# Optimization experiments

Measured on AMD Instinct MI355X. Metric: run time of the kernel, lower is better.

The kernel has to match this reference:

```python
import jax, jax.numpy as jnp
import numpy as np
from jax import lax

B, N, C = 8, 2000, 81
MAX_INST = 100
MIN_CONF = 0.7
NMS_THR = 0.3
WINDOW = jnp.array([0.0, 0.0, 1.0, 1.0], jnp.float32)  # y1, x1, y2, x2
BBOX_STD = jnp.array([0.1, 0.1, 0.2, 0.2], jnp.float32)


def setup_inputs() -> dict:
    key = jax.random.key(0)
    k1, k2, k3 = jax.random.split(key, 3)
    # build valid boxes: sample coordinate pairs and sort so y1<=y2, x1<=x2
    yx = jax.random.uniform(k1, (B, N, 2, 2), dtype=jnp.float32)
    mins, maxs = yx.min(axis=2), yx.max(axis=2)
    rois = jnp.stack([mins[..., 0], mins[..., 1], maxs[..., 0], maxs[..., 1]], axis=-1)
    probs = jax.random.uniform(k2, (B, N, C), dtype=jnp.float32)
    deltas = jax.random.normal(k3, (B, N, C, 4), dtype=jnp.float32) * 0.5
    return {"rois": rois, "probs": probs, "deltas": deltas}


def _apply_box_deltas(boxes, deltas):
    # boxes: [N,4] (y1,x1,y2,x2); deltas: [N,4] (dy,dx,log_dh,log_dw)
    h = boxes[:, 2] - boxes[:, 0]
    w = boxes[:, 3] - boxes[:, 1]
    cy = boxes[:, 0] + 0.5 * h + deltas[:, 0] * h
    cx = boxes[:, 1] + 0.5 * w + deltas[:, 1] * w
    h = h * jnp.exp(deltas[:, 2])
    w = w * jnp.exp(deltas[:, 3])
    return jnp.stack([cy - 0.5 * h, cx - 0.5 * w, cy + 0.5 * h, cx + 0.5 * w], axis=1)


def _clip_boxes(boxes, window):
    wy1, wx1, wy2, wx2 = window
    y1 = jnp.clip(boxes[:, 0], wy1, wy2)
    x1 = jnp.clip(boxes[:, 1], wx1, wx2)
    y2 = jnp.clip(boxes[:, 2], wy1, wy2)
    x2 = jnp.clip(boxes[:, 3], wx1, wx2)
    return jnp.stack([y1, x1, y2, x2], axis=1)


def _pairwise_iou(boxes):
    # boxes: [N,4] -> [N,N]
    y1, x1, y2, x2 = boxes[:, 0], boxes[:, 1], boxes[:, 2], boxes[:, 3]
    area = (y2 - y1) * (x2 - x1)
    iy1 = jnp.maximum(y1[:, None], y1[None, :])
    ix1 = jnp.maximum(x1[:, None], x1[None, :])
    iy2 = jnp.minimum(y2[:, None], y2[None, :])
    ix2 = jnp.minimum(x2[:, None], x2[None, :])
    inter = jnp.maximum(iy2 - iy1, 0.0) * jnp.maximum(ix2 - ix1, 0.0)
    union = area[:, None] + area[None, :] - inter
    return inter / jnp.maximum(union, 1e-12)


def _refine_one(rois, probs, deltas):
    # rois [N,4], probs [N,C], deltas [N,C,4]
    class_ids = jnp.argmax(probs, axis=1)                      # [N]
    rng = jnp.arange(N)
    class_scores = probs[rng, class_ids]                       # [N]
    deltas_specific = deltas[rng, class_ids]                   # [N,4]
    refined = _apply_box_deltas(rois, deltas_specific * BBOX_STD)
    refined = _clip_boxes(refined, WINDOW)

    valid = (class_ids > 0) & (class_scores >= MIN_CONF)

    # sort by score descending (invalid entries pushed to the end)
    order = jnp.argsort(-jnp.where(valid, class_scores, -jnp.inf))
    boxes_s = refined[order]
    scores_s = class_scores[order]
    cls_s = class_ids[order]
    valid_s = valid[order]

    # per-class greedy NMS: suppress only within the same class
    iou = _pairwise_iou(boxes_s)                               # [N,N]
    suppress_mat = (iou > NMS_THR) & (cls_s[:, None] == cls_s[None, :])
    lower = jnp.arange(N)

    def body(i, keep):
        sup = suppress_mat[i] & keep[i] & (lower > i)
        return keep & ~sup

    keep = lax.fori_loop(0, N, body, valid_s)

    # per-class cap at MAX_INST (mirrors max_output_size in tf NMS)
    onehot = jax.nn.one_hot(cls_s, C, dtype=jnp.int32) * keep.astype(jnp.int32)[:, None]
    rank = jnp.cumsum(onehot, axis=0)[lower, cls_s]            # inclusive per-class rank
    keep = keep & (rank <= MAX_INST)

    # global top-k by score among kept, zero-padded
    final_scores = jnp.where(keep, scores_s, -jnp.inf)
    _, top_idx = lax.top_k(final_scores, MAX_INST)
    valid_top = keep[top_idx]
    box_out = jnp.where(valid_top[:, None], boxes_s[top_idx], 0.0)
    cls_out = jnp.where(valid_top, cls_s[top_idx].astype(jnp.float32), 0.0)
    sc_out = jnp.where(valid_top, scores_s[top_idx], 0.0)
    return jnp.concatenate([box_out, cls_out[:, None], sc_out[:, None]], axis=1)  # [MAX_INST,6]


def reference(rois, probs, deltas):
    return jax.vmap(_refine_one)(rois, probs, deltas)  # [B, MAX_INST, 6]
```

## Files before the change

kernel.cpp:

```cpp
#include <hip/hip_runtime.h>
#include <math.h>

#define BB 8
#define NN 2000
#define CC 81
#define NCLS 80
#define MAXI 100
#define MCLS 128
#define WCAP 128

static constexpr float kMinConf = 0.7f;
static constexpr float kNmsThr  = 0.3f;


__device__ __forceinline__ unsigned long long mkey(float s, int i) {
    return ((unsigned long long)__float_as_uint(s) << 32) | (unsigned int)(~(unsigned int)i);
}

__device__ __forceinline__ bool iou_gt_thr(float4 a, float aarea, float4 t) {
    float iy1 = fmaxf(a.x, t.x), ix1 = fmaxf(a.y, t.y);
    float iy2 = fminf(a.z, t.z), ix2 = fminf(a.w, t.w);
    float inter = fmaxf(iy2 - iy1, 0.f) * fmaxf(ix2 - ix1, 0.f);
    float tarea = (t.z - t.x) * (t.w - t.y);
    float uni = fmaxf(aarea + tarea - inter, 1e-12f);
    return inter > kNmsThr * uni;
}

__global__ void kA_refine(const float* __restrict__ rois,
                          const float* __restrict__ probs,
                          const float* __restrict__ deltas,
                          float* __restrict__ boxes,
                          float* __restrict__ sc,
                          int* __restrict__ cls,
                          int* __restrict__ kflag,
                          float* __restrict__ outz) {
    int gtid = blockIdx.x * blockDim.x + threadIdx.x;
    if (gtid < BB * MAXI * 6) outz[gtid] = 0.f;
    if (gtid < BB * NN) kflag[gtid] = 0;

    int wid = gtid >> 6;
    int l = gtid & 63;

    const float* p = probs + (size_t)wid * CC;
    float v1 = p[l];
    int   i1 = l;
    int   c2 = l + 64;
    float v2 = (c2 < CC) ? p[c2] : -1.0f;
    float bv; int bi;
    if (v2 > v1) { bv = v2; bi = c2; } else { bv = v1; bi = i1; }

    #pragma unroll
    for (int off = 32; off; off >>= 1) {
        float ov = __shfl_xor(bv, off);
        int   oi = __shfl_xor(bi, off);
        if (ov > bv || (ov == bv && oi < bi)) { bv = ov; bi = oi; }
    }

    if (l == 0) {
        const float4 dl = *(const float4*)(deltas + ((size_t)wid * CC + bi) * 4);
        float dy = dl.x * 0.1f, dx = dl.y * 0.1f, dh = dl.z * 0.2f, dw = dl.w * 0.2f;
        const float4 r = *(const float4*)(rois + (size_t)wid * 4);
        float y1 = r.x, x1 = r.y, y2 = r.z, x2 = r.w;
        float h = y2 - y1, w = x2 - x1;
        float cy = y1 + 0.5f * h + dy * h;
        float cx = x1 + 0.5f * w + dx * w;
        float h2 = h * expf(dh);
        float w2 = w * expf(dw);
        float oy1 = fminf(fmaxf(cy - 0.5f * h2, 0.f), 1.f);
        float ox1 = fminf(fmaxf(cx - 0.5f * w2, 0.f), 1.f);
        float oy2 = fminf(fmaxf(cy + 0.5f * h2, 0.f), 1.f);
        float ox2 = fminf(fmaxf(cx + 0.5f * w2, 0.f), 1.f);
        bool valid = (bi > 0) && (bv >= kMinConf);
        float4 bx; bx.x = oy1; bx.y = ox1; bx.z = oy2; bx.w = ox2;
        ((float4*)boxes)[wid] = bx;
        sc[wid] = bv;
        cls[wid] = valid ? bi : 0;
    }
}

__global__ void __launch_bounds__(256) kB_nms(
        const float* __restrict__ boxes,
        const float* __restrict__ sc,
        const int* __restrict__ cls,
        int* __restrict__ kflag) {
    const int p = blockIdx.x;
    const int b = p / NCLS;
    const int cidx = p % NCLS;
    const int c = cidx + 1;
    const int tid = threadIdx.x;
    const int wv = tid >> 6;
    const int l = tid & 63;

    __shared__ unsigned long long wlist[4][WCAP];
    __shared__ int wcnt[4];
    __shared__ unsigned long long mk[MCLS];
    __shared__ float4 mbox[MCLS];

    const int* cl = cls + (size_t)b * NN;
    const float* ssc = sc + (size_t)b * NN;
    const float4* bxs = (const float4*)boxes + (size_t)b * NN;

    {
        int cnt = 0;
        const int base_row = wv * 500;
        for (int ch = 0; ch < 8; ++ch) {
            int idx = ch * 64 + l;
            bool inq = idx < 500;
            int r = base_row + idx;
            int ci = inq ? cl[r] : 0;
            bool pred = (ci == c);
            unsigned long long mask = __ballot(pred);
            if (pred) {
                int pos = cnt + __popcll(mask & ((1ull << l) - 1ull));
                if (pos < WCAP) wlist[wv][pos] = mkey(ssc[r], r);
            }
            cnt += __popcll(mask);
        }
        if (l == 0) wcnt[wv] = (cnt > WCAP) ? WCAP : cnt;
    }
    __syncthreads();

    int b0 = wcnt[0], b1 = wcnt[1], b2 = wcnt[2], b3 = wcnt[3];
    int myofs = (wv > 0 ? b0 : 0) + (wv > 1 ? b1 : 0) + (wv > 2 ? b2 : 0);
    int myn = wcnt[wv];
    int cnt_all = b0 + b1 + b2 + b3;
    if (cnt_all > MCLS) cnt_all = MCLS;
    if (l < myn && myofs + l < MCLS) mk[myofs + l] = wlist[wv][l];
    if (64 + l < myn && myofs + 64 + l < MCLS) mk[myofs + 64 + l] = wlist[wv][64 + l];
    __syncthreads();

    if (wv != 0) return;
    if (cnt_all == 0) return;
    const int cnt = cnt_all;

    {
        unsigned long long Ka = (l < cnt) ? mk[l] : 0ull;
        unsigned long long Kb = (64 + l < cnt) ? mk[64 + l] : 0ull;
        int ra = 0, rb = 0;
        for (int t = 0; t < cnt; ++t) {
            unsigned long long kt = mk[t];
            ra += (kt > Ka);
            rb += (kt > Kb);
        }
        if (l < cnt) mk[ra] = Ka;
        if (64 + l < cnt) mk[rb] = Kb;
    }

    for (int t = l; t < cnt; t += 64) {
        int i = (int)(~(unsigned int)mk[t]);
        mbox[t] = bxs[i];
    }

    unsigned long long kept0 = 0ull;
    {
        bool act = (l < cnt);
        float4 a = mbox[act ? l : 0];
        float aarea = (a.z - a.x) * (a.w - a.y);
        unsigned long long colmask = 0ull;
        int tend = min(64, cnt);
        for (int t = 0; t < tend; ++t) {
            float4 tb = mbox[t];
            if (t < l && act && iou_gt_thr(a, aarea, tb)) colmask |= (1ull << t);
        }
        unsigned long long kept = __ballot(act);
        while (true) {
            bool alive = act && ((colmask & kept) == 0ull);
            unsigned long long k2m = __ballot(alive);
            if (k2m == kept) break;
            kept = k2m;
        }
        kept0 = kept;
        bool alive = act && ((colmask & kept0) == 0ull);
        if (alive) kflag[(size_t)b * NN + (int)(~(unsigned int)mk[l])] = 1;
    }
    if (cnt > 64) {
        int m = 64 + l;
        bool act = (m < cnt);
        float4 a = mbox[act ? m : 0];
        float aarea = (a.z - a.x) * (a.w - a.y);
        bool presup = false;
        for (int t = 0; t < 64; ++t) {
            if ((kept0 >> t) & 1ull) {
                if (act && iou_gt_thr(a, aarea, mbox[t])) presup = true;
            }
        }
        unsigned long long colmask = 0ull;
        for (int t = 64; t < cnt; ++t) {
            float4 tb = mbox[t];
            if ((t - 64) < l && act && iou_gt_thr(a, aarea, tb)) colmask |= (1ull << (t - 64));
        }
        bool pre = act && !presup;
        unsigned long long kept = __ballot(pre);
        while (true) {
            bool alive = pre && ((colmask & kept) == 0ull);
            unsigned long long k2m = __ballot(alive);
            if (k2m == kept) break;
            kept = k2m;
        }
        bool alive = pre && ((colmask & kept) == 0ull);
        if (alive) kflag[(size_t)b * NN + (int)(~(unsigned int)mk[64 + l])] = 1;
    }
}

__global__ void __launch_bounds__(1024) kC_emit(
        const int* __restrict__ kflag,
        const float* __restrict__ sc,
        const float* __restrict__ boxes,
        const int* __restrict__ cls,
        float* __restrict__ out) {
    const int b = blockIdx.x;
    const int tid = threadIdx.x;
    const int wv = tid >> 6;
    const int l = tid & 63;

    __shared__ unsigned long long keys[2048];
    __shared__ ulonglong2 cand2[256];
    __shared__ int hist[256];
    __shared__ int Tcnt, tbsh, candn;
    unsigned long long* cand = (unsigned long long*)cand2;

    if (tid < 256) hist[tid] = 0;
    if (tid < 48) keys[2000 + tid] = 0ull;
    if (tid == 0) { Tcnt = 0; candn = 0; }
    __syncthreads();

    for (int i = tid; i < NN; i += 1024) {
        int f = kflag[(size_t)b * NN + i];
        unsigned long long k = f ? mkey(sc[(size_t)b * NN + i], i) : 0ull;
        keys[i] = k;
        if (f) atomicAdd(&hist[(int)((k >> 47) & 0xFF)], 1);
        unsigned long long m = __ballot(f != 0);
        if (l == 0 && m) atomicAdd(&Tcnt, __popcll(m));
    }
    __syncthreads();
    const int T = Tcnt;
    if (T == 0) return;

    if (wv == 0) {
        int cum = 0, tb = 0, done = 0;
        for (int chunk = 3; chunk >= 0 && !done; --chunk) {
            int bkt = chunk * 64 + (63 - l);
            int s = hist[bkt];
            #pragma unroll
            for (int off = 1; off < 64; off <<= 1) {
                int o = __shfl_up(s, off);
                if (l >= off) s += o;
            }
            int chunktot = __shfl(s, 63);
            if (cum + chunktot >= MAXI) {
                unsigned long long m = __ballot(cum + s >= MAXI);
                int lane = __ffsll((long long)m) - 1;
                tb = chunk * 64 + (63 - lane);
                done = 1;
            } else {
                cum += chunktot;
            }
        }
        if (l == 0) tbsh = done ? tb : 0;
    }
    __syncthreads();
    const int tb = tbsh;

    for (int i = tid; i < NN; i += 1024) {
        unsigned long long k = keys[i];
        bool pr = (k != 0ull) && ((int)((k >> 47) & 0xFF) >= tb);
        unsigned long long m = __ballot(pr);
        int basew = 0;
        if (l == 0 && m) basew = atomicAdd(&candn, __popcll(m));
        basew = __shfl(basew, 0);
        if (pr) {
            int pos = basew + __popcll(m & ((1ull << l) - 1ull));
            if (pos < 512) cand[pos] = k;
        }
    }
    __syncthreads();
    const int nc = candn;
    if (tid == 0 && nc < 512) cand[nc] = 0ull;
    __syncthreads();

    if (nc <= 512) {
        const int np = (nc + 1) >> 1;
        for (int s = tid; s < nc; s += 1024) {
            unsigned long long myk = cand[s];
            int r = 0;
            for (int t = 0; t < np; ++t) {
                ulonglong2 kv = cand2[t];
                r += (int)(kv.x > myk);
                r += (int)(kv.y > myk);
            }
            if (r < MAXI) {
                int i = (int)(~(unsigned int)myk);
                float4 bx = ((const float4*)boxes)[(size_t)b * NN + i];
                float* o = out + ((size_t)b * MAXI + r) * 6;
                o[0] = bx.x; o[1] = bx.y; o[2] = bx.z; o[3] = bx.w;
                o[4] = (float)cls[(size_t)b * NN + i];
                o[5] = __uint_as_float((unsigned int)(myk >> 32));
            }
        }
    } else {
        for (int s = tid; s < NN; s += 1024) {
            unsigned long long myk = keys[s];
            if (myk == 0ull) continue;
            int r = 0;
            for (int t = 0; t < 1024; ++t) {
                ulonglong2 kv = ((ulonglong2*)keys)[t];
                r += (int)(kv.x > myk);
                r += (int)(kv.y > myk);
            }
            if (r < MAXI) {
                int i = (int)(~(unsigned int)myk);
                float4 bx = ((const float4*)boxes)[(size_t)b * NN + i];
                float* o = out + ((size_t)b * MAXI + r) * 6;
                o[0] = bx.x; o[1] = bx.y; o[2] = bx.z; o[3] = bx.w;
                o[4] = (float)cls[(size_t)b * NN + i];
                o[5] = __uint_as_float((unsigned int)(myk >> 32));
            }
        }
    }
}

extern "C" void kernel_launch(void* const* d_in, const int* in_sizes, int n_in,
                              void* d_out, int out_size, void* d_ws, size_t ws_size,
                              hipStream_t stream) {
    const float* rois   = (const float*)d_in[0];
    const float* probs  = (const float*)d_in[1];
    const float* deltas = (const float*)d_in[2];
    float* outp = (float*)d_out;

    char* ws = (char*)d_ws;
    float* boxes = (float*)(ws + 0);
    float* sc    = (float*)(ws + 256000);
    int*   cls   = (int*)  (ws + 320000);
    int*   kflag = (int*)  (ws + 384000);

    {
        int blocks = (BB * NN * 64) / 256;
        kA_refine<<<blocks, 256, 0, stream>>>(rois, probs, deltas, boxes, sc, cls, kflag, outp);
    }
    {
        kB_nms<<<BB * NCLS, 256, 0, stream>>>(boxes, sc, cls, kflag);
    }
    {
        kC_emit<<<BB, 1024, 0, stream>>>(kflag, sc, boxes, cls, outp);
    }
}
```

Measured before the change: 29.09 us.

## Bucket detections per class via atomics and fuse NMS with emit kernel

The refine kernel now appends each valid detection's score/index key into per-class slot lists using atomic counters. This replaces the NMS kernel's full scan of class ids. NMS and top-k emission are fused into one 1024-thread block per batch, with 16 wavefronts each handling 5 classes and writing kept keys straight into shared memory instead of a global flag array. This removes a kernel launch and global round-trips, but adds a memset, atomic contention, and far fewer blocks (8 instead of 640) for the NMS work.

```diff
diff --git a/kernel.cpp b/kernel.cpp
--- a/kernel.cpp
+++ b/kernel.cpp
@@ -7,7 +7,6 @@
 #define NCLS 80
 #define MAXI 100
 #define MCLS 128
-#define WCAP 128
 
 static constexpr float kMinConf = 0.7f;
 static constexpr float kNmsThr  = 0.3f;
@@ -30,13 +29,12 @@
                           const float* __restrict__ probs,
                           const float* __restrict__ deltas,
                           float* __restrict__ boxes,
-                          float* __restrict__ sc,
                           int* __restrict__ cls,
-                          int* __restrict__ kflag,
+                          int* __restrict__ ccnt,
+                          unsigned long long* __restrict__ cslot,
                           float* __restrict__ outz) {
     int gtid = blockIdx.x * blockDim.x + threadIdx.x;
     if (gtid < BB * MAXI * 6) outz[gtid] = 0.f;
-    if (gtid < BB * NN) kflag[gtid] = 0;
 
     int wid = gtid >> 6;
     int l = gtid & 63;
@@ -73,170 +71,136 @@
         bool valid = (bi > 0) && (bv >= kMinConf);
         float4 bx; bx.x = oy1; bx.y = ox1; bx.z = oy2; bx.w = ox2;
         ((float4*)boxes)[wid] = bx;
-        sc[wid] = bv;
         cls[wid] = valid ? bi : 0;
-    }
-}
-
-__global__ void __launch_bounds__(256) kB_nms(
+        if (valid) {
+            int b = wid / NN, i = wid - b * NN;
+            int cidx = bi - 1;
+            int pos = atomicAdd(&ccnt[b * NCLS + cidx], 1);
+            if (pos < MCLS)
+                cslot[(size_t)(b * NCLS + cidx) * MCLS + pos] = mkey(bv, i);
+        }
+    }
+}
+
+__global__ void __launch_bounds__(1024) k2_nms_emit(
         const float* __restrict__ boxes,
-        const float* __restrict__ sc,
         const int* __restrict__ cls,
-        int* __restrict__ kflag) {
-    const int p = blockIdx.x;
-    const int b = p / NCLS;
-    const int cidx = p % NCLS;
-    const int c = cidx + 1;
+        const int* __restrict__ ccnt,
+        const unsigned long long* __restrict__ cslot,
+        float* __restrict__ out) {
+    const int b = blockIdx.x;
     const int tid = threadIdx.x;
-    const int wv = tid >> 6;
+    const int w = tid >> 6;
     const int l = tid & 63;
 
-    __shared__ unsigned long long wlist[4][WCAP];
-    __shared__ int wcnt[4];
-    __shared__ unsigned long long mk[MCLS];
-    __shared__ float4 mbox[MCLS];
-
-    const int* cl = cls + (size_t)b * NN;
-    const float* ssc = sc + (size_t)b * NN;
+    __shared__ unsigned long long mk16[16][MCLS];
+    __shared__ float4 mbox16[16][64];
+    __shared__ ulonglong2 keys2[1024];
+    __shared__ ulonglong2 cand2[256];
+    __shared__ int hist[256];
+    __shared__ int ccl[NCLS];
+    __shared__ int Tcnt, tbsh, candn;
+    unsigned long long* keys = (unsigned long long*)keys2;
+    unsigned long long* cand = (unsigned long long*)cand2;
+
+    for (int i = tid; i < 2048; i += 1024) keys[i] = 0ull;
+    if (tid < NCLS) ccl[tid] = min(ccnt[b * NCLS + tid], MCLS);
+    if (tid < 256) hist[tid] = 0;
+    if (tid == 0) { Tcnt = 0; candn = 0; }
+    __syncthreads();
+
     const float4* bxs = (const float4*)boxes + (size_t)b * NN;
-
-    {
-        int cnt = 0;
-        const int base_row = wv * 500;
-        for (int ch = 0; ch < 8; ++ch) {
-            int idx = ch * 64 + l;
-            bool inq = idx < 500;
-            int r = base_row + idx;
-            int ci = inq ? cl[r] : 0;
-            bool pred = (ci == c);
-            unsigned long long mask = __ballot(pred);
-            if (pred) {
-                int pos = cnt + __popcll(mask & ((1ull << l) - 1ull));
-                if (pos < WCAP) wlist[wv][pos] = mkey(ssc[r], r);
-            }
-            cnt += __popcll(mask);
-        }
-        if (l == 0) wcnt[wv] = (cnt > WCAP) ? WCAP : cnt;
-    }
-    __syncthreads();
-
-    int b0 = wcnt[0], b1 = wcnt[1], b2 = wcnt[2], b3 = wcnt[3];
-    int myofs = (wv > 0 ? b0 : 0) + (wv > 1 ? b1 : 0) + (wv > 2 ? b2 : 0);
-    int myn = wcnt[wv];
-    int cnt_all = b0 + b1 + b2 + b3;
-    if (cnt_all > MCLS) cnt_all = MCLS;
-    if (l < myn && myofs + l < MCLS) mk[myofs + l] = wlist[wv][l];
-    if (64 + l < myn && myofs + 64 + l < MCLS) mk[myofs + 64 + l] = wlist[wv][64 + l];
-    __syncthreads();
-
-    if (wv != 0) return;
-    if (cnt_all == 0) return;
-    const int cnt = cnt_all;
-
-    {
-        unsigned long long Ka = (l < cnt) ? mk[l] : 0ull;
-        unsigned long long Kb = (64 + l < cnt) ? mk[64 + l] : 0ull;
+    unsigned long long* mk = mk16[w];
+    float4* mbox = mbox16[w];
+
+    for (int k = 0; k < 5; ++k) {
+        const int cidx = w + 16 * k;
+        const int cnt = ccl[cidx];
+        if (cnt == 0) continue;
+        const unsigned long long* slot = cslot + (size_t)(b * NCLS + cidx) * MCLS;
+
+        unsigned long long va = (l < cnt) ? slot[l] : 0ull;
+        unsigned long long vb = (64 + l < cnt) ? slot[64 + l] : 0ull;
+        if (l < cnt) mk[l] = va;
+        if (64 + l < cnt) mk[64 + l] = vb;
         int ra = 0, rb = 0;
         for (int t = 0; t < cnt; ++t) {
             unsigned long long kt = mk[t];
-            ra += (kt > Ka);
-            rb += (kt > Kb);
-        }
-        if (l < cnt) mk[ra] = Ka;
-        if (64 + l < cnt) mk[rb] = Kb;
-    }
-
-    for (int t = l; t < cnt; t += 64) {
-        int i = (int)(~(unsigned int)mk[t]);
-        mbox[t] = bxs[i];
-    }
-
-    unsigned long long kept0 = 0ull;
-    {
-        bool act = (l < cnt);
-        float4 a = mbox[act ? l : 0];
-        float aarea = (a.z - a.x) * (a.w - a.y);
-        unsigned long long colmask = 0ull;
-        int tend = min(64, cnt);
-        for (int t = 0; t < tend; ++t) {
-            float4 tb = mbox[t];
-            if (t < l && act && iou_gt_thr(a, aarea, tb)) colmask |= (1ull << t);
-        }
-        unsigned long long kept = __ballot(act);
-        while (true) {
-            bool alive = act && ((colmask & kept) == 0ull);
-            unsigned long long k2m = __ballot(alive);
-            if (k2m == kept) break;
-            kept = k2m;
-        }
-        kept0 = kept;
-        bool alive = act && ((colmask & kept0) == 0ull);
-        if (alive) kflag[(size_t)b * NN + (int)(~(unsigned int)mk[l])] = 1;
-    }
-    if (cnt > 64) {
-        int m = 64 + l;
-        bool act = (m < cnt);
-        float4 a = mbox[act ? m : 0];
-        float aarea = (a.z - a.x) * (a.w - a.y);
-        bool presup = false;
-        for (int t = 0; t < 64; ++t) {
-            if ((kept0 >> t) & 1ull) {
-                if (act && iou_gt_thr(a, aarea, mbox[t])) presup = true;
-            }
-        }
-        unsigned long long colmask = 0ull;
-        for (int t = 64; t < cnt; ++t) {
-            float4 tb = mbox[t];
-            if ((t - 64) < l && act && iou_gt_thr(a, aarea, tb)) colmask |= (1ull << (t - 64));
-        }
-        bool pre = act && !presup;
-        unsigned long long kept = __ballot(pre);
-        while (true) {
+            ra += (kt > va);
+            rb += (kt > vb);
+        }
+        if (l < cnt) mk[ra] = va;
+        if (64 + l < cnt) mk[rb] = vb;
+
+        if (l < min(cnt, 64)) mbox[l] = bxs[(int)(~(unsigned int)mk[l])];
+
+        unsigned long long kept0 = 0ull;
+        {
+            bool act = (l < cnt);
+            float4 a = mbox[act ? l : 0];
+            float aarea = (a.z - a.x) * (a.w - a.y);
+            unsigned long long colmask = 0ull;
+            int tend = min(64, cnt);
+            for (int t = 0; t < tend; ++t) {
+                float4 tb = mbox[t];
+                if (t < l && act && iou_gt_thr(a, aarea, tb)) colmask |= (1ull << t);
+            }
+            unsigned long long kept = __ballot(act);
+            while (true) {
+                bool alive = act && ((colmask & kept) == 0ull);
+                unsigned long long k2m = __ballot(alive);
+                if (k2m == kept) break;
+                kept = k2m;
+            }
+            kept0 = kept;
+            bool alive = act && ((colmask & kept0) == 0ull);
+            if (alive) keys[(int)(~(unsigned int)mk[l])] = mk[l];
+        }
+        if (cnt > 64) {
+            int m = 64 + l;
+            bool act = (m < cnt);
+            unsigned long long myk = act ? mk[m] : 0ull;
+            float4 a = act ? bxs[(int)(~(unsigned int)myk)]
+                           : make_float4(0.f, 0.f, 0.f, 0.f);
+            float aarea = (a.z - a.x) * (a.w - a.y);
+            bool presup = false;
+            for (int t = 0; t < 64; ++t) {
+                if ((kept0 >> t) & 1ull) {
+                    if (act && iou_gt_thr(a, aarea, mbox[t])) presup = true;
+                }
+            }
+            unsigned long long colmask = 0ull;
+            for (int t = 64; t < cnt; ++t) {
+                float4 tb = bxs[(int)(~(unsigned int)mk[t])];
+                if ((t - 64) < l && act && iou_gt_thr(a, aarea, tb))
+                    colmask |= (1ull << (t - 64));
+            }
+            bool pre = act && !presup;
+            unsigned long long kept = __ballot(pre);
+            while (true) {
+                bool alive = pre && ((colmask & kept) == 0ull);
+                unsigned long long k2m = __ballot(alive);
+                if (k2m == kept) break;
+                kept = k2m;
+            }
             bool alive = pre && ((colmask & kept) == 0ull);
-            unsigned long long k2m = __ballot(alive);
-            if (k2m == kept) break;
-            kept = k2m;
-        }
-        bool alive = pre && ((colmask & kept) == 0ull);
-        if (alive) kflag[(size_t)b * NN + (int)(~(unsigned int)mk[64 + l])] = 1;
-    }
-}
-
-__global__ void __launch_bounds__(1024) kC_emit(
-        const int* __restrict__ kflag,
-        const float* __restrict__ sc,
-        const float* __restrict__ boxes,
-        const int* __restrict__ cls,
-        float* __restrict__ out) {
-    const int b = blockIdx.x;
-    const int tid = threadIdx.x;
-    const int wv = tid >> 6;
-    const int l = tid & 63;
-
-    __shared__ unsigned long long keys[2048];
-    __shared__ ulonglong2 cand2[256];
-    __shared__ int hist[256];
-    __shared__ int Tcnt, tbsh, candn;
-    unsigned long long* cand = (unsigned long long*)cand2;
-
-    if (tid < 256) hist[tid] = 0;
-    if (tid < 48) keys[2000 + tid] = 0ull;
-    if (tid == 0) { Tcnt = 0; candn = 0; }
+            if (alive) keys[(int)(~(unsigned int)myk)] = myk;
+        }
+    }
     __syncthreads();
 
     for (int i = tid; i < NN; i += 1024) {
-        int f = kflag[(size_t)b * NN + i];
-        unsigned long long k = f ? mkey(sc[(size_t)b * NN + i], i) : 0ull;
-        keys[i] = k;
-        if (f) atomicAdd(&hist[(int)((k >> 47) & 0xFF)], 1);
-        unsigned long long m = __ballot(f != 0);
+        unsigned long long kv = keys[i];
+        bool f = (kv != 0ull);
+        if (f) atomicAdd(&hist[(int)((kv >> 47) & 0xFF)], 1);
+        unsigned long long m = __ballot(f);
         if (l == 0 && m) atomicAdd(&Tcnt, __popcll(m));
     }
     __syncthreads();
     const int T = Tcnt;
     if (T == 0) return;
 
-    if (wv == 0) {
+    if (w == 0) {
         int cum = 0, tb = 0, done = 0;
         for (int chunk = 3; chunk >= 0 && !done; --chunk) {
             int bkt = chunk * 64 + (63 - l);
@@ -262,15 +226,15 @@
     const int tb = tbsh;
 
     for (int i = tid; i < NN; i += 1024) {
-        unsigned long long k = keys[i];
-        bool pr = (k != 0ull) && ((int)((k >> 47) & 0xFF) >= tb);
+        unsigned long long kv = keys[i];
+        bool pr = (kv != 0ull) && ((int)((kv >> 47) & 0xFF) >= tb);
         unsigned long long m = __ballot(pr);
         int basew = 0;
         if (l == 0 && m) basew = atomicAdd(&candn, __popcll(m));
         basew = __shfl(basew, 0);
         if (pr) {
             int pos = basew + __popcll(m & ((1ull << l) - 1ull));
-            if (pos < 512) cand[pos] = k;
+            if (pos < 512) cand[pos] = kv;
         }
     }
     __syncthreads();
@@ -290,7 +254,7 @@
             }
             if (r < MAXI) {
                 int i = (int)(~(unsigned int)myk);
-                float4 bx = ((const float4*)boxes)[(size_t)b * NN + i];
+                float4 bx = bxs[i];
                 float* o = out + ((size_t)b * MAXI + r) * 6;
                 o[0] = bx.x; o[1] = bx.y; o[2] = bx.z; o[3] = bx.w;
                 o[4] = (float)cls[(size_t)b * NN + i];
@@ -303,13 +267,13 @@
             if (myk == 0ull) continue;
             int r = 0;
             for (int t = 0; t < 1024; ++t) {
-                ulonglong2 kv = ((ulonglong2*)keys)[t];
+                ulonglong2 kv = keys2[t];
                 r += (int)(kv.x > myk);
                 r += (int)(kv.y > myk);
             }
             if (r < MAXI) {
                 int i = (int)(~(unsigned int)myk);
-                float4 bx = ((const float4*)boxes)[(size_t)b * NN + i];
+                float4 bx = bxs[i];
                 float* o = out + ((size_t)b * MAXI + r) * 6;
                 o[0] = bx.x; o[1] = bx.y; o[2] = bx.z; o[3] = bx.w;
                 o[4] = (float)cls[(size_t)b * NN + i];
@@ -329,18 +293,17 @@
 
     char* ws = (char*)d_ws;
     float* boxes = (float*)(ws + 0);
-    float* sc    = (float*)(ws + 256000);
-    int*   cls   = (int*)  (ws + 320000);
-    int*   kflag = (int*)  (ws + 384000);
-
+    int*   cls   = (int*)  (ws + 256000);
+    int*   ccnt  = (int*)  (ws + 320000);
+    unsigned long long* cslot = (unsigned long long*)(ws + 322560);
+
+    hipMemsetAsync(ccnt, 0, BB * NCLS * sizeof(int), stream);
     {
         int blocks = (BB * NN * 64) / 256;
-        kA_refine<<<blocks, 256, 0, stream>>>(rois, probs, deltas, boxes, sc, cls, kflag, outp);
+        kA_refine<<<blocks, 256, 0, stream>>>(rois, probs, deltas, boxes, cls,
+                                              ccnt, cslot, outp);
     }
     {
-        kB_nms<<<BB * NCLS, 256, 0, stream>>>(boxes, sc, cls, kflag);
-    }
-    {
-        kC_emit<<<BB, 1024, 0, stream>>>(kflag, sc, boxes, cls, outp);
-    }
-}
+        k2_nms_emit<<<BB, 1024, 0, stream>>>(boxes, cls, ccnt, cslot, outp);
+    }
+}
```

Result: slower. 68.18 us (+134.4%).

## Store sort keys from NMS and split emit kernel across 32 blocks per batch

Applied to the files above, without the earlier changes.

The NMS kernel now writes the full 64-bit score/index key for each surviving box instead of a flag, so the emit kernel no longer rebuilds keys from scores. The emit kernel goes from one 1024-thread block per batch to 32 blocks of 256 threads per batch. Every block repeats the histogram and candidate selection, but each block only ranks and writes candidates whose index falls in its residue class mod 32. This spreads the rank-counting work over more CUs, at the cost of redundant per-block scanning and twice the key-buffer traffic.

```diff
diff --git a/kernel.cpp b/kernel.cpp
--- a/kernel.cpp
+++ b/kernel.cpp
@@ -32,11 +32,11 @@
                           float* __restrict__ boxes,
                           float* __restrict__ sc,
                           int* __restrict__ cls,
-                          int* __restrict__ kflag,
+                          unsigned long long* __restrict__ keysrc,
                           float* __restrict__ outz) {
     int gtid = blockIdx.x * blockDim.x + threadIdx.x;
     if (gtid < BB * MAXI * 6) outz[gtid] = 0.f;
-    if (gtid < BB * NN) kflag[gtid] = 0;
+    if (gtid < BB * NN) keysrc[gtid] = 0ull;
 
     int wid = gtid >> 6;
     int l = gtid & 63;
@@ -82,7 +82,7 @@
         const float* __restrict__ boxes,
         const float* __restrict__ sc,
         const int* __restrict__ cls,
-        int* __restrict__ kflag) {
+        unsigned long long* __restrict__ keysrc) {
     const int p = blockIdx.x;
     const int b = p / NCLS;
     const int cidx = p % NCLS;
@@ -171,7 +171,10 @@
         }
         kept0 = kept;
         bool alive = act && ((colmask & kept0) == 0ull);
-        if (alive) kflag[(size_t)b * NN + (int)(~(unsigned int)mk[l])] = 1;
+        if (alive) {
+            unsigned long long myk = mk[l];
+            keysrc[(size_t)b * NN + (int)(~(unsigned int)myk)] = myk;
+        }
     }
     if (cnt > 64) {
         int m = 64 + l;
@@ -198,38 +201,44 @@
             kept = k2m;
         }
         bool alive = pre && ((colmask & kept) == 0ull);
-        if (alive) kflag[(size_t)b * NN + (int)(~(unsigned int)mk[64 + l])] = 1;
-    }
-}
-
-__global__ void __launch_bounds__(1024) kC_emit(
-        const int* __restrict__ kflag,
-        const float* __restrict__ sc,
+        if (alive) {
+            unsigned long long myk = mk[64 + l];
+            keysrc[(size_t)b * NN + (int)(~(unsigned int)myk)] = myk;
+        }
+    }
+}
+
+__global__ void __launch_bounds__(256) kC_emit(
+        const unsigned long long* __restrict__ keysrc,
         const float* __restrict__ boxes,
         const int* __restrict__ cls,
         float* __restrict__ out) {
-    const int b = blockIdx.x;
+    const int b = blockIdx.x >> 5;
+    const int q = blockIdx.x & 31;
     const int tid = threadIdx.x;
     const int wv = tid >> 6;
     const int l = tid & 63;
 
-    __shared__ unsigned long long keys[2048];
+    __shared__ ulonglong2 keys2[1024];
     __shared__ ulonglong2 cand2[256];
     __shared__ int hist[256];
     __shared__ int Tcnt, tbsh, candn;
+    unsigned long long* keys = (unsigned long long*)keys2;
     unsigned long long* cand = (unsigned long long*)cand2;
 
-    if (tid < 256) hist[tid] = 0;
+    hist[tid] = 0;
     if (tid < 48) keys[2000 + tid] = 0ull;
     if (tid == 0) { Tcnt = 0; candn = 0; }
     __syncthreads();
 
-    for (int i = tid; i < NN; i += 1024) {
-        int f = kflag[(size_t)b * NN + i];
-        unsigned long long k = f ? mkey(sc[(size_t)b * NN + i], i) : 0ull;
-        keys[i] = k;
-        if (f) atomicAdd(&hist[(int)((k >> 47) & 0xFF)], 1);
-        unsigned long long m = __ballot(f != 0);
+    const float4* bxs = (const float4*)boxes + (size_t)b * NN;
+
+    for (int i = tid; i < NN; i += 256) {
+        unsigned long long kv = keysrc[(size_t)b * NN + i];
+        keys[i] = kv;
+        bool f = (kv != 0ull);
+        if (f) atomicAdd(&hist[(int)((kv >> 47) & 0xFF)], 1);
+        unsigned long long m = __ballot(f);
         if (l == 0 && m) atomicAdd(&Tcnt, __popcll(m));
     }
     __syncthreads();
@@ -261,16 +270,16 @@
     __syncthreads();
     const int tb = tbsh;
 
-    for (int i = tid; i < NN; i += 1024) {
-        unsigned long long k = keys[i];
-        bool pr = (k != 0ull) && ((int)((k >> 47) & 0xFF) >= tb);
+    for (int i = tid; i < NN; i += 256) {
+        unsigned long long kv = keys[i];
+        bool pr = (kv != 0ull) && ((int)((kv >> 47) & 0xFF) >= tb);
         unsigned long long m = __ballot(pr);
         int basew = 0;
         if (l == 0 && m) basew = atomicAdd(&candn, __popcll(m));
         basew = __shfl(basew, 0);
         if (pr) {
             int pos = basew + __popcll(m & ((1ull << l) - 1ull));
-            if (pos < 512) cand[pos] = k;
+            if (pos < 512) cand[pos] = kv;
         }
     }
     __syncthreads();
@@ -280,8 +289,10 @@
 
     if (nc <= 512) {
         const int np = (nc + 1) >> 1;
-        for (int s = tid; s < nc; s += 1024) {
+        for (int s = tid; s < nc; s += 256) {
             unsigned long long myk = cand[s];
+            int i = (int)(~(unsigned int)myk);
+            if ((i & 31) != q) continue;
             int r = 0;
             for (int t = 0; t < np; ++t) {
                 ulonglong2 kv = cand2[t];
@@ -289,8 +300,7 @@
                 r += (int)(kv.y > myk);
             }
             if (r < MAXI) {
-                int i = (int)(~(unsigned int)myk);
-                float4 bx = ((const float4*)boxes)[(size_t)b * NN + i];
+                float4 bx = bxs[i];
                 float* o = out + ((size_t)b * MAXI + r) * 6;
                 o[0] = bx.x; o[1] = bx.y; o[2] = bx.z; o[3] = bx.w;
                 o[4] = (float)cls[(size_t)b * NN + i];
@@ -298,21 +308,21 @@
             }
         }
     } else {
-        for (int s = tid; s < NN; s += 1024) {
+        for (int s = tid; s < NN; s += 256) {
             unsigned long long myk = keys[s];
             if (myk == 0ull) continue;
+            if ((s & 31) != q) continue;
             int r = 0;
             for (int t = 0; t < 1024; ++t) {
-                ulonglong2 kv = ((ulonglong2*)keys)[t];
+                ulonglong2 kv = keys2[t];
                 r += (int)(kv.x > myk);
                 r += (int)(kv.y > myk);
             }
             if (r < MAXI) {
-                int i = (int)(~(unsigned int)myk);
-                float4 bx = ((const float4*)boxes)[(size_t)b * NN + i];
+                float4 bx = bxs[s];
                 float* o = out + ((size_t)b * MAXI + r) * 6;
                 o[0] = bx.x; o[1] = bx.y; o[2] = bx.z; o[3] = bx.w;
-                o[4] = (float)cls[(size_t)b * NN + i];
+                o[4] = (float)cls[(size_t)b * NN + s];
                 o[5] = __uint_as_float((unsigned int)(myk >> 32));
             }
         }
@@ -331,16 +341,13 @@
     float* boxes = (float*)(ws + 0);
     float* sc    = (float*)(ws + 256000);
     int*   cls   = (int*)  (ws + 320000);
-    int*   kflag = (int*)  (ws + 384000);
+    unsigned long long* keysrc = (unsigned long long*)(ws + 384000);
 
     {
         int blocks = (BB * NN * 64) / 256;
-        kA_refine<<<blocks, 256, 0, stream>>>(rois, probs, deltas, boxes, sc, cls, kflag, outp);
-    }
-    {
-        kB_nms<<<BB * NCLS, 256, 0, stream>>>(boxes, sc, cls, kflag);
-    }
-    {
-        kC_emit<<<BB, 1024, 0, stream>>>(kflag, sc, boxes, cls, outp);
-    }
-}
+        kA_refine<<<blocks, 256, 0, stream>>>(rois, probs, deltas, boxes, sc,
+                                              cls, keysrc, outp);
+    }
+    kB_nms<<<BB * NCLS, 256, 0, stream>>>(boxes, sc, cls, keysrc);
+    kC_emit<<<BB * 32, 256, 0, stream>>>(keysrc, boxes, cls, outp);
+}
```

Result: slower. 38.48 us (+32.3%).
